# Kernel tuning notes

Hardware: AMD Instinct MI355X
Metric: run time of the kernel (lower is better)

The kernel has to match this reference:

```python
import jax, jax.numpy as jnp
import numpy as np

N = 100000   # nodes
E = 1600000  # edges
D = 256      # emb_dim
H = 512      # 2*emb_dim hidden in GIN MLP
L = 5        # num_layer
NUM_NODE_TYPES = 300
EDGE_FEAT = 7


def setup_inputs() -> dict:
    key = jax.random.key(0)
    ks = jax.random.split(key, 16)
    s = 0.05
    return {
        "x": jax.random.randint(ks[0], (N, 1), 0, NUM_NODE_TYPES, dtype=jnp.int32),
        "edge_index": jax.random.randint(ks[1], (2, E), 0, N, dtype=jnp.int32),
        "edge_attr": jax.random.normal(ks[2], (E, EDGE_FEAT), dtype=jnp.float32),
        "batch": jnp.zeros((N,), dtype=jnp.int32),
        "node_emb": jax.random.normal(ks[3], (NUM_NODE_TYPES, D), dtype=jnp.float32) * s,
        "We": jax.random.normal(ks[4], (L, EDGE_FEAT, D), dtype=jnp.float32) * s,
        "be": jnp.zeros((L, D), dtype=jnp.float32),
        "W1": jax.random.normal(ks[5], (L, D, H), dtype=jnp.float32) * s,
        "b1": jnp.zeros((L, H), dtype=jnp.float32),
        "g1": jnp.ones((L, H), dtype=jnp.float32),
        "bt1": jnp.zeros((L, H), dtype=jnp.float32),
        "W2": jax.random.normal(ks[6], (L, H, D), dtype=jnp.float32) * s,
        "b2": jnp.zeros((L, D), dtype=jnp.float32),
        "eps": jnp.zeros((L,), dtype=jnp.float32),
        "g_bn": jnp.ones((L, D), dtype=jnp.float32),
        "b_bn": jnp.zeros((L, D), dtype=jnp.float32),
    }


def _batchnorm(z, g, b):
    # training-mode BN over the node dim, biased variance, eps=1e-5 (torch default)
    mu = jnp.mean(z, axis=0)
    var = jnp.mean((z - mu) ** 2, axis=0)
    return (z - mu) * jax.lax.rsqrt(var + 1e-5) * g + b


def reference(x, edge_index, edge_attr, batch, node_emb, We, be, W1, b1, g1, bt1,
              W2, b2, eps, g_bn, b_bn):
    src, dst = edge_index[0], edge_index[1]
    h = node_emb[x[:, 0]]                      # [N, D]
    n = h.shape[0]
    for l in range(L):
        edge_emb = edge_attr @ We[l] + be[l]   # [E, D]
        msg = jax.nn.relu(h[src] + edge_emb)   # gather + elementwise message
        agg = jax.ops.segment_sum(msg, dst, num_segments=n)  # scatter-add
        z = (1.0 + eps[l]) * h + agg
        z = jax.nn.relu(_batchnorm(z @ W1[l] + b1[l], g1[l], bt1[l])) @ W2[l] + b2[l]
        z = _batchnorm(z, g_bn[l], b_bn[l])
        h = jax.nn.relu(z) if l != L - 1 else z  # relu on all but last; dropout p=0
    return h  # JK='last'
```

## Files before the change

### kernel.cpp

```cpp
#include <hip/hip_runtime.h>
#include <hip/hip_bf16.h>

#define N_NODES 100000
#define N_EDGES 1600000
#define DIM 256
#define HID 512
#define NLAYERS 5
#define MTILES 782

typedef unsigned short u16;
typedef unsigned int u32;
typedef short s16x8 __attribute__((ext_vector_type(8)));
typedef float f32x4 __attribute__((ext_vector_type(4)));

__device__ __forceinline__ float b2f_(u16 u) {
  union { unsigned i; float f; } v;
  v.i = ((unsigned)u) << 16;
  return v.f;
}
__device__ __forceinline__ u16 f2b_(float f) {
  __hip_bfloat16 h = __float2bfloat16(f);
  return *reinterpret_cast<u16*>(&h);
}
__device__ __forceinline__ int pk2_(u16 lo, u16 hi) {
  return (int)(((u32)hi << 16) | (u32)lo);
}
__device__ __forceinline__ int4 bn_pack_(int4 raw, const float* __restrict__ scl,
                                         const float* __restrict__ sft) {
  const u16* rp = (const u16*)&raw;
  u16 o[8];
#pragma unroll
  for (int q = 0; q < 8; ++q) {
    float v = fmaf(b2f_(rp[q]), scl[q], sft[q]);
    o[q] = f2b_(fmaxf(v, 0.f));
  }
  return make_int4(pk2_(o[0], o[1]), pk2_(o[2], o[3]), pk2_(o[4], o[5]), pk2_(o[6], o[7]));
}

__device__ __forceinline__ void gl16_(const u16* g, u16* l) {
  __builtin_amdgcn_global_load_lds(
      (const __attribute__((address_space(1))) void*)g,
      (__attribute__((address_space(3))) void*)l, 16, 0, 0);
}

__device__ __forceinline__ int lds_off(int row, int g) {
  return row * 32 + (((g ^ (row >> 1)) & 3) << 3);
}

__global__ void k_fill(float* out, int n, float val) {
  int i = blockIdx.x * 256 + threadIdx.x;
  if (i < n) out[i] = val;
}

__global__ void k_zero(float* p, int n) {
  int i = blockIdx.x * 256 + threadIdx.x;
  if (i < n) p[i] = 0.f;
}

__global__ void k_zeroi(int* p, int n) {
  int i = blockIdx.x * 256 + threadIdx.x;
  if (i < n) p[i] = 0;
}

__global__ void k_gather(const int* x0, const int* x3, const float* emb, float* h) {
  int idx = blockIdx.x * 256 + threadIdx.x;
  int n = idx >> 8, d = idx & 255;
  int t = x0[n] + x3[n];
  h[idx] = emb[(size_t)t * DIM + d];
}

__global__ void k_hist(const int* __restrict__ dst, int* __restrict__ deg) {
  int e = blockIdx.x * 256 + threadIdx.x;
  if (e < N_EDGES) atomicAdd(&deg[dst[e]], 1);
}

__global__ void k_scan1(const int* __restrict__ deg, int* __restrict__ offs,
                        int* __restrict__ bsum) {
  __shared__ int sm[256];
  int tid = threadIdx.x;
  int i = blockIdx.x * 256 + tid;
  int v = (i < N_NODES) ? deg[i] : 0;
  sm[tid] = v;
  __syncthreads();
  for (int d = 1; d < 256; d <<= 1) {
    int t = (tid >= d) ? sm[tid - d] : 0;
    __syncthreads();
    sm[tid] += t;
    __syncthreads();
  }
  if (i < N_NODES) offs[i] = sm[tid] - v;
  if (tid == 0) bsum[blockIdx.x] = sm[255];
}

__global__ void k_scan2(int* __restrict__ bsum, int nb) {
  __shared__ int sm[512];
  int tid = threadIdx.x;
  int v = (tid < nb) ? bsum[tid] : 0;
  sm[tid] = v;
  __syncthreads();
  for (int d = 1; d < 512; d <<= 1) {
    int t = (tid >= d) ? sm[tid - d] : 0;
    __syncthreads();
    sm[tid] += t;
    __syncthreads();
  }
  if (tid < nb) bsum[tid] = sm[tid] - v;
}

__global__ void k_scan3(int* __restrict__ offs, const int* __restrict__ bsum,
                        int* __restrict__ cur) {
  int i = blockIdx.x * 256 + threadIdx.x;
  if (i < N_NODES) {
    offs[i] += bsum[blockIdx.x];
    cur[i] = 0;
  }
  if (i == 0) offs[N_NODES] = N_EDGES;
}

__global__ void k_fillcsr(const int* __restrict__ dst, const int* __restrict__ srcarr,
                          const float* __restrict__ ea, const int* __restrict__ offs,
                          int* __restrict__ cur, int* __restrict__ elist,
                          float* __restrict__ eaperm) {
  int e = blockIdx.x * 256 + threadIdx.x;
  if (e < N_EDGES) {
    int d = dst[e];
    int p = offs[d] + atomicAdd(&cur[d], 1);
    elist[p] = srcarr[e];
    const float* s = ea + (size_t)e * 7;
    float* o = eaperm + (size_t)p * 7;
#pragma unroll
    for (int k = 0; k < 7; ++k) o[k] = s[k];
  }
}

template <int BNIN>
__global__ __launch_bounds__(256) void k_agg(
    const float* __restrict__ hin, const float* __restrict__ eap,
    const int* __restrict__ csr, const int* __restrict__ offs,
    const float* __restrict__ We, const float* __restrict__ be,
    const float* __restrict__ eps_l, const float* __restrict__ scl2,
    const float* __restrict__ sft2, u16* __restrict__ zh, u16* __restrict__ zl) {
  const int lane = threadIdx.x & 63;
  const int n = blockIdx.x * 4 + (threadIdx.x >> 6);
  const int c0 = lane * 4;
  float w[7][4];
#pragma unroll
  for (int k = 0; k < 7; ++k) {
    f32x4 t = *(const f32x4*)&We[k * DIM + c0];
    w[k][0] = t[0]; w[k][1] = t[1]; w[k][2] = t[2]; w[k][3] = t[3];
  }
  const f32x4 bev = *(const f32x4*)&be[c0];
  f32x4 sv, fv;
  if (BNIN) { sv = *(const f32x4*)&scl2[c0]; fv = *(const f32x4*)&sft2[c0]; }
  const f32x4 hn = *(const f32x4*)&hin[(size_t)n * DIM + c0];
  const float e1p = 1.0f + eps_l[0];
  float acc[4];
#pragma unroll
  for (int q = 0; q < 4; ++q) {
    float hv = hn[q];
    if (BNIN) hv = fmaxf(fmaf(hv, sv[q], fv[q]), 0.f);
    acc[q] = e1p * hv;
  }

  auto msg = [&](const f32x4& hs, const float* a) {
#pragma unroll
    for (int q = 0; q < 4; ++q) {
      float hv = hs[q];
      if (BNIN) hv = fmaxf(fmaf(hv, sv[q], fv[q]), 0.f);
      float t = bev[q];
#pragma unroll
      for (int k = 0; k < 7; ++k) t = fmaf(a[k], w[k][q], t);
      acc[q] += fmaxf(hv + t, 0.f);
    }
  };

  const int eb = offs[n], ee = offs[n + 1];
  for (int base = eb; base < ee; base += 64) {
    const int m = min(64, ee - base);
    const int cs = csr[base + min(lane, m - 1)];
    int e = 0;
    for (; e + 4 <= m; e += 4) {
      const int s0 = __shfl(cs, e);
      const int s1 = __shfl(cs, e + 1);
      const int s2 = __shfl(cs, e + 2);
      const int s3 = __shfl(cs, e + 3);
      const f32x4 h0 = *(const f32x4*)&hin[(size_t)s0 * DIM + c0];
      const f32x4 h1 = *(const f32x4*)&hin[(size_t)s1 * DIM + c0];
      const f32x4 h2 = *(const f32x4*)&hin[(size_t)s2 * DIM + c0];
      const f32x4 h3 = *(const f32x4*)&hin[(size_t)s3 * DIM + c0];
      const float* p0 = eap + (size_t)(base + e) * 7;
      float a0[7], a1[7], a2[7], a3[7];
#pragma unroll
      for (int k = 0; k < 7; ++k) {
        a0[k] = p0[k]; a1[k] = p0[7 + k]; a2[k] = p0[14 + k]; a3[k] = p0[21 + k];
      }
      msg(h0, a0);
      msg(h1, a1);
      msg(h2, a2);
      msg(h3, a3);
    }
    for (; e < m; ++e) {
      const int s0 = __shfl(cs, e);
      const f32x4 h0 = *(const f32x4*)&hin[(size_t)s0 * DIM + c0];
      const float* p0 = eap + (size_t)(base + e) * 7;
      float a0[7];
#pragma unroll
      for (int k = 0; k < 7; ++k) a0[k] = p0[k];
      msg(h0, a0);
    }
  }
  ushort4 zh4, zl4;
#pragma unroll
  for (int q = 0; q < 4; ++q) {
    u16 hh = f2b_(acc[q]);
    float lo = acc[q] - b2f_(hh);
    ((u16*)&zh4)[q] = hh;
    ((u16*)&zl4)[q] = f2b_(lo);
  }
  *(ushort4*)&zh[(size_t)n * DIM + c0] = zh4;
  *(ushort4*)&zl[(size_t)n * DIM + c0] = zl4;
}

template <int K, int NC>
__global__ void k_wconv(const float* __restrict__ W, u16* __restrict__ Wth,
                        u16* __restrict__ Wtl) {
  int idx = blockIdx.x * 256 + threadIdx.x;
  int n = idx / K, k = idx - n * K;
  float w = W[(size_t)k * NC + n];
  u16 hh = f2b_(w);
  Wth[idx] = hh;
  Wtl[idx] = f2b_(w - b2f_(hh));
}

__global__ void k_bnprep(const float* __restrict__ sum, const float* __restrict__ sq,
                         const float* __restrict__ g, const float* __restrict__ bt,
                         float* __restrict__ scl, float* __restrict__ sft, int n) {
  int j = blockIdx.x * 256 + threadIdx.x;
  if (j < n) {
    const float invN = 1.0f / 100000.0f;
    float mu = sum[j] * invN;
    float var = fmaf(-mu, mu, sq[j] * invN);
    float s = g[j] * rsqrtf(var + 1e-5f);
    scl[j] = s;
    sft[j] = fmaf(-mu, s, bt[j]);
  }
}

template <int K, int NC, int NA, int OBF, int BN1A>
__global__ __launch_bounds__(256) void k_mgemm(
    const u16* __restrict__ Ah, const u16* __restrict__ Al,
    const u16* __restrict__ Bth, const u16* __restrict__ Btl,
    const float* __restrict__ bias, void* __restrict__ Ov,
    float* __restrict__ colsum, float* __restrict__ colsq,
    const float* __restrict__ ascl, const float* __restrict__ asft) {
  __shared__ u16 As[NA * 128 * 32];
  __shared__ u16 Bs[2 * 128 * 32];
  constexpr int NT = NC / 128;
  const int nwg = MTILES * NT;
  const int bid = blockIdx.x;
  const int q = nwg >> 3, r = nwg & 7;
  const int xcd = bid & 7, pos = bid >> 3;
  const int lidx = (xcd < r) ? (xcd * (q + 1) + pos)
                             : (r * (q + 1) + (xcd - r) * q + pos);
  const int mt = lidx / NT;
  const int m0 = mt * 128;
  const int n0 = (lidx - mt * NT) * 128;

  const int tid = threadIdx.x;
  const int lane = tid & 63;
  const int wv = tid >> 6;
  const int wr = (wv >> 1) * 64;
  const int wc = (wv & 1) * 64;
  const int lr = lane & 15;
  const int g = lane >> 4;
  const int sr = tid >> 1;
  const int sc = (tid & 1) * 16;
  const int ga = min(m0 + sr, N_NODES - 1);
  const int grow16 = lane >> 2;
  const int glc = (lane & 3) ^ ((lane >> 3) & 3);

  const f32x4 z4 = {0.f, 0.f, 0.f, 0.f};
  f32x4 acc[4][4];
#pragma unroll
  for (int i = 0; i < 4; ++i)
#pragma unroll
    for (int j = 0; j < 4; ++j) acc[i][j] = z4;

  for (int k0 = 0; k0 < K; k0 += 32) {
    int4 a0, a1;
    if (NA == 1) {
      const u16* srcp = Ah + (size_t)ga * K + k0 + sc;
      a0 = *(const int4*)(srcp);
      a1 = *(const int4*)(srcp + 8);
      if (BN1A) {
        a0 = bn_pack_(a0, ascl + k0 + sc, asft + k0 + sc);
        a1 = bn_pack_(a1, ascl + k0 + sc + 8, asft + k0 + sc + 8);
      }
    }
    __syncthreads();
    if (NA == 2) {
      const u16* gbase;
      u16* lbase;
      int rbase, rclamp;
      if (wv == 0)      { gbase = Ah;  lbase = As;        rbase = m0; rclamp = N_NODES - 1; }
      else if (wv == 1) { gbase = Al;  lbase = As + 4096; rbase = m0; rclamp = N_NODES - 1; }
      else if (wv == 2) { gbase = Bth; lbase = Bs;        rbase = n0; rclamp = 0x7fffffff; }
      else              { gbase = Btl; lbase = Bs + 4096; rbase = n0; rclamp = 0x7fffffff; }
#pragma unroll
      for (int c = 0; c < 8; ++c) {
        int gr = min(rbase + c * 16 + grow16, rclamp);
        gl16_(gbase + (size_t)gr * K + k0 + glc * 8, lbase + c * 512);
      }
    } else {
      const int x = (sr >> 1) & 3;
      const int lc0 = (tid & 1) * 2;
      *(int4*)&As[sr * 32 + ((lc0 ^ x) << 3)] = a0;
      *(int4*)&As[sr * 32 + (((lc0 + 1) ^ x) << 3)] = a1;
      const u16* gbase = (wv >> 1) ? Btl : Bth;
      u16* lbase = (wv >> 1) ? Bs + 4096 : Bs;
#pragma unroll
      for (int cc = 0; cc < 4; ++cc) {
        int c = (wv & 1) * 4 + cc;
        int gr = n0 + c * 16 + grow16;
        gl16_(gbase + (size_t)gr * K + k0 + glc * 8, lbase + c * 512);
      }
    }
    __syncthreads();

    s16x8 aF[NA][4], bF[2][4];
#pragma unroll
    for (int i = 0; i < 4; ++i) {
      aF[0][i] = *reinterpret_cast<const s16x8*>(&As[lds_off(wr + i * 16 + lr, g)]);
      if (NA == 2)
        aF[1][i] = *reinterpret_cast<const s16x8*>(&As[4096 + lds_off(wr + i * 16 + lr, g)]);
      bF[0][i] = *reinterpret_cast<const s16x8*>(&Bs[lds_off(wc + i * 16 + lr, g)]);
      bF[1][i] = *reinterpret_cast<const s16x8*>(&Bs[4096 + lds_off(wc + i * 16 + lr, g)]);
    }
#pragma unroll
    for (int i = 0; i < 4; ++i)
#pragma unroll
      for (int j = 0; j < 4; ++j) {
        acc[i][j] =
            __builtin_amdgcn_mfma_f32_16x16x32_bf16(aF[0][i], bF[0][j], acc[i][j], 0, 0, 0);
        acc[i][j] =
            __builtin_amdgcn_mfma_f32_16x16x32_bf16(aF[0][i], bF[1][j], acc[i][j], 0, 0, 0);
        if (NA == 2)
          acc[i][j] =
              __builtin_amdgcn_mfma_f32_16x16x32_bf16(aF[1][i], bF[0][j], acc[i][j], 0, 0, 0);
      }
  }

  float bj[4];
#pragma unroll
  for (int j = 0; j < 4; ++j) bj[j] = bias[n0 + wc + j * 16 + lr];
  float ls[4] = {0.f, 0.f, 0.f, 0.f}, lq[4] = {0.f, 0.f, 0.f, 0.f};
#pragma unroll
  for (int i = 0; i < 4; ++i) {
    const int row0 = m0 + wr + i * 16 + (lane >> 4) * 4;
#pragma unroll
    for (int r2 = 0; r2 < 4; ++r2) {
      const int grow = row0 + r2;
      if (grow < N_NODES) {
        const size_t o = (size_t)grow * NC + n0 + wc + lr;
#pragma unroll
        for (int j = 0; j < 4; ++j) {
          float v = acc[i][j][r2] + bj[j];
          ls[j] += v;
          lq[j] = fmaf(v, v, lq[j]);
          if (OBF) ((u16*)Ov)[o + j * 16] = f2b_(v);
          else ((float*)Ov)[o + j * 16] = v;
        }
      }
    }
  }
#pragma unroll
  for (int j = 0; j < 4; ++j) {
    float s = ls[j], q2 = lq[j];
    s += __shfl_xor(s, 16); q2 += __shfl_xor(q2, 16);
    s += __shfl_xor(s, 32); q2 += __shfl_xor(q2, 32);
    if ((lane >> 4) == 0) {
      unsafeAtomicAdd(&colsum[n0 + wc + j * 16 + lr], s);
      unsafeAtomicAdd(&colsq[n0 + wc + j * 16 + lr], q2);
    }
  }
}

__global__ void k_bn(const void* Y, int y_bf, const float* sum, const float* sq,
                     const float* g, const float* b, int NC_mask,
                     void* O, int o_bf, int do_relu) {
  int idx = blockIdx.x * 256 + threadIdx.x;
  int j = idx & NC_mask;
  const float invN = 1.0f / 100000.0f;
  float mu = sum[j] * invN;
  float var = fmaf(-mu, mu, sq[j] * invN);
  float v = y_bf ? b2f_(((const u16*)Y)[idx]) : ((const float*)Y)[idx];
  v = fmaf((v - mu) * rsqrtf(var + 1e-5f), g[j], b[j]);
  if (do_relu) v = fmaxf(v, 0.f);
  if (o_bf) ((u16*)O)[idx] = f2b_(v);
  else ((float*)O)[idx] = v;
}

extern "C" void kernel_launch(void* const* d_in, const int* in_sizes, int n_in,
                              void* d_out, int out_size, void* d_ws, size_t ws_size,
                              hipStream_t stream) {
  float* out = (float*)d_out;

  const int expected[16] = {100000, 3200000, 11200000, 100000, 76800, 8960, 1280,
                            655360, 2560, 2560, 2560, 655360, 1280, 5, 1280, 1280};
  float sentinel = 0.f;
  if (n_in != 16) sentinel = 60.f;
  else
    for (int i = 0; i < 16; ++i)
      if (in_sizes[i] != expected[i]) { sentinel = 100.f + (float)i; break; }
  if (sentinel == 0.f && out_size != N_NODES * DIM) sentinel = 90.f;

  const size_t ND = (size_t)N_NODES * DIM;
  const size_t NH = (size_t)N_NODES * HID;
  const size_t base = 4096 * sizeof(float);
  const size_t need_base = base + 2 * ND * sizeof(float) + NH * sizeof(u16);
  if (sentinel == 0.f && ws_size < need_base) sentinel = 77.f;
  if (sentinel != 0.f) {
    k_fill<<<(out_size + 255) / 256, 256, 0, stream>>>(out, out_size, sentinel);
    return;
  }

  float* stats = (float*)d_ws;
  float* sum1 = stats;
  float* sq1 = sum1 + HID;
  float* sum2 = sq1 + HID;
  float* sq2 = sum2 + DIM;
  float* scl1 = stats + 1536;
  float* sft1 = scl1 + HID;
  float* scl2 = sft1 + HID;
  float* sft2 = scl2 + DIM;
  float* bufA = stats + 4096;
  float* bufB = bufA + ND;
  u16* Y1 = (u16*)(bufB + ND);

  const size_t csr_ints =
      (size_t)N_NODES + (size_t)(N_NODES + 1) + 512 + 1 + (size_t)N_EDGES;
  const size_t csr_bytes = csr_ints * sizeof(int) + (size_t)N_EDGES * 7 * sizeof(float);
  const int csr_tail = ws_size >= need_base + csr_bytes;
  int* degc = csr_tail ? (int*)((char*)d_ws + need_base) : (int*)Y1;
  int* offs = degc + N_NODES;
  int* bsum = offs + N_NODES + 1;
  int* elist = bsum + 512 + 1;
  float* eaperm = (float*)(elist + N_EDGES);
  const int NB_N = (N_NODES + 255) / 256;
  const int NB_E = N_EDGES / 256;

  const int* x0 = (const int*)d_in[0];
  const int* ei = (const int*)d_in[1];
  const float* ea = (const float*)d_in[2];
  const int* x3 = (const int*)d_in[3];
  const float* emb = (const float*)d_in[4];
  const float* We = (const float*)d_in[5];
  const float* be = (const float*)d_in[6];
  const float* W1 = (const float*)d_in[7];
  const float* b1 = (const float*)d_in[8];
  const float* g1 = (const float*)d_in[9];
  const float* bt1 = (const float*)d_in[10];
  const float* W2 = (const float*)d_in[11];
  const float* b2 = (const float*)d_in[12];
  const float* eps = (const float*)d_in[13];
  const float* g_bn = (const float*)d_in[14];
  const float* b_bn = (const float*)d_in[15];

  const int* srcs = ei;
  const int* dsts = ei + N_EDGES;

  const int gridND = (int)(ND / 256);

  auto build_csr = [&]() {
    k_zeroi<<<NB_N, 256, 0, stream>>>(degc, N_NODES);
    k_hist<<<NB_E, 256, 0, stream>>>(dsts, degc);
    k_scan1<<<NB_N, 256, 0, stream>>>(degc, offs, bsum);
    k_scan2<<<1, 512, 0, stream>>>(bsum, NB_N);
    k_scan3<<<NB_N, 256, 0, stream>>>(offs, bsum, degc);
    k_fillcsr<<<NB_E, 256, 0, stream>>>(dsts, srcs, ea, offs, degc, elist, eaperm);
  };

  k_gather<<<gridND, 256, 0, stream>>>(x0, x3, emb, bufA);
  if (csr_tail) build_csr();

  float* bufs[2] = {bufA, bufB};
  int p = 0;
  for (int l = 0; l < NLAYERS; ++l) {
    float* IN = bufs[p];
    float* ZB = bufs[1 - p];
    u16* zh = (u16*)ZB;
    u16* zl = zh + ND;
    u16* Wth = (u16*)IN;
    u16* Wtl = Wth + (size_t)DIM * HID;

    if (!csr_tail) build_csr();
    k_zero<<<6, 256, 0, stream>>>(stats, 1536);

    if (l == 0)
      k_agg<0><<<N_NODES / 4, 256, 0, stream>>>(IN, eaperm, elist, offs,
                                                We + (size_t)l * 7 * DIM,
                                                be + (size_t)l * DIM, eps + l,
                                                nullptr, nullptr, zh, zl);
    else
      k_agg<1><<<N_NODES / 4, 256, 0, stream>>>(IN, eaperm, elist, offs,
                                                We + (size_t)l * 7 * DIM,
                                                be + (size_t)l * DIM, eps + l,
                                                scl2, sft2, zh, zl);

    k_wconv<DIM, HID><<<(DIM * HID) / 256, 256, 0, stream>>>(
        W1 + (size_t)l * DIM * HID, Wth, Wtl);
    k_mgemm<DIM, HID, 2, 1, 0><<<MTILES * (HID / 128), 256, 0, stream>>>(
        zh, zl, Wth, Wtl, b1 + (size_t)l * HID, Y1, sum1, sq1, nullptr, nullptr);
    k_bnprep<<<2, 256, 0, stream>>>(sum1, sq1, g1 + (size_t)l * HID,
                                    bt1 + (size_t)l * HID, scl1, sft1, HID);

    k_wconv<HID, DIM><<<(DIM * HID) / 256, 256, 0, stream>>>(
        W2 + (size_t)l * HID * DIM, Wth, Wtl);
    k_mgemm<HID, DIM, 1, 0, 1><<<MTILES * (DIM / 128), 256, 0, stream>>>(
        Y1, nullptr, Wth, Wtl, b2 + (size_t)l * DIM, ZB, sum2, sq2, scl1, sft1);

    if (l != NLAYERS - 1)
      k_bnprep<<<1, 256, 0, stream>>>(sum2, sq2, g_bn + (size_t)l * DIM,
                                      b_bn + (size_t)l * DIM, scl2, sft2, DIM);
    else
      k_bn<<<gridND, 256, 0, stream>>>(ZB, 0, sum2, sq2, g_bn + (size_t)l * DIM,
                                       b_bn + (size_t)l * DIM, DIM - 1, out, 0, 0);
    p ^= 1;
  }
}
```

Baseline: 2.878 ms.

## Double-buffer LDS tiles in split-bf16 MFMA GEMM to overlap loads with compute

Restructures the GEMM k-loop to use two LDS buffers for A and B tiles. The next tile's global-to-LDS DMA and register loads are issued before the current tile's MFMAs, so memory latency can hide behind compute. This also drops one barrier per iteration. In exchange the kernel uses twice the shared memory, which can lower occupancy, and holds more live registers across the MFMA block.

```diff
diff --git a/kernel.cpp b/kernel.cpp
--- a/kernel.cpp
+++ b/kernel.cpp
@@ -253,18 +253,20 @@
     const float* __restrict__ bias, void* __restrict__ Ov,
     float* __restrict__ colsum, float* __restrict__ colsq,
     const float* __restrict__ ascl, const float* __restrict__ asft) {
-  __shared__ u16 As[NA * 128 * 32];
-  __shared__ u16 Bs[2 * 128 * 32];
-  constexpr int NT = NC / 128;
-  const int nwg = MTILES * NT;
+  constexpr int PL = 128 * 32;
+  constexpr int NT = K / 32;
+  __shared__ u16 As[2 * NA * PL];
+  __shared__ u16 Bs[2 * 2 * PL];
+  constexpr int NTL = NC / 128;
+  const int nwg = MTILES * NTL;
   const int bid = blockIdx.x;
   const int q = nwg >> 3, r = nwg & 7;
   const int xcd = bid & 7, pos = bid >> 3;
   const int lidx = (xcd < r) ? (xcd * (q + 1) + pos)
                              : (r * (q + 1) + (xcd - r) * q + pos);
-  const int mt = lidx / NT;
+  const int mt = lidx / NTL;
   const int m0 = mt * 128;
-  const int n0 = (lidx - mt * NT) * 128;
+  const int n0 = (lidx - mt * NTL) * 128;
 
   const int tid = threadIdx.x;
   const int lane = tid & 63;
@@ -279,45 +281,24 @@
   const int grow16 = lane >> 2;
   const int glc = (lane & 3) ^ ((lane >> 3) & 3);
 
-  const f32x4 z4 = {0.f, 0.f, 0.f, 0.f};
-  f32x4 acc[4][4];
-#pragma unroll
-  for (int i = 0; i < 4; ++i)
-#pragma unroll
-    for (int j = 0; j < 4; ++j) acc[i][j] = z4;
-
-  for (int k0 = 0; k0 < K; k0 += 32) {
-    int4 a0, a1;
-    if (NA == 1) {
-      const u16* srcp = Ah + (size_t)ga * K + k0 + sc;
-      a0 = *(const int4*)(srcp);
-      a1 = *(const int4*)(srcp + 8);
-      if (BN1A) {
-        a0 = bn_pack_(a0, ascl + k0 + sc, asft + k0 + sc);
-        a1 = bn_pack_(a1, ascl + k0 + sc + 8, asft + k0 + sc + 8);
-      }
-    }
-    __syncthreads();
+  auto stage_dma = [&](int kt, int buf) {
+    const int k0 = kt * 32;
     if (NA == 2) {
       const u16* gbase;
       u16* lbase;
       int rbase, rclamp;
-      if (wv == 0)      { gbase = Ah;  lbase = As;        rbase = m0; rclamp = N_NODES - 1; }
-      else if (wv == 1) { gbase = Al;  lbase = As + 4096; rbase = m0; rclamp = N_NODES - 1; }
-      else if (wv == 2) { gbase = Bth; lbase = Bs;        rbase = n0; rclamp = 0x7fffffff; }
-      else              { gbase = Btl; lbase = Bs + 4096; rbase = n0; rclamp = 0x7fffffff; }
+      if (wv == 0)      { gbase = Ah;  lbase = As + buf * (NA * PL);      rbase = m0; rclamp = N_NODES - 1; }
+      else if (wv == 1) { gbase = Al;  lbase = As + buf * (NA * PL) + PL; rbase = m0; rclamp = N_NODES - 1; }
+      else if (wv == 2) { gbase = Bth; lbase = Bs + buf * (2 * PL);       rbase = n0; rclamp = 0x7fffffff; }
+      else              { gbase = Btl; lbase = Bs + buf * (2 * PL) + PL;  rbase = n0; rclamp = 0x7fffffff; }
 #pragma unroll
       for (int c = 0; c < 8; ++c) {
         int gr = min(rbase + c * 16 + grow16, rclamp);
         gl16_(gbase + (size_t)gr * K + k0 + glc * 8, lbase + c * 512);
       }
     } else {
-      const int x = (sr >> 1) & 3;
-      const int lc0 = (tid & 1) * 2;
-      *(int4*)&As[sr * 32 + ((lc0 ^ x) << 3)] = a0;
-      *(int4*)&As[sr * 32 + (((lc0 + 1) ^ x) << 3)] = a1;
       const u16* gbase = (wv >> 1) ? Btl : Bth;
-      u16* lbase = (wv >> 1) ? Bs + 4096 : Bs;
+      u16* lbase = Bs + buf * (2 * PL) + ((wv >> 1) ? PL : 0);
 #pragma unroll
       for (int cc = 0; cc < 4; ++cc) {
         int c = (wv & 1) * 4 + cc;
@@ -325,16 +306,60 @@
         gl16_(gbase + (size_t)gr * K + k0 + glc * 8, lbase + c * 512);
       }
     }
-    __syncthreads();
-
+  };
+  auto a_write = [&](int4 a0, int4 a1, int buf) {
+    const int x = (sr >> 1) & 3;
+    const int lc0 = (tid & 1) * 2;
+    u16* ab = As + buf * PL;
+    *(int4*)&ab[sr * 32 + ((lc0 ^ x) << 3)] = a0;
+    *(int4*)&ab[sr * 32 + (((lc0 + 1) ^ x) << 3)] = a1;
+  };
+  auto a_load = [&](int kt, int4& a0, int4& a1) {
+    const u16* srcp = Ah + (size_t)ga * K + kt * 32 + sc;
+    a0 = *(const int4*)(srcp);
+    a1 = *(const int4*)(srcp + 8);
+  };
+  auto a_bn = [&](int4& a0, int4& a1, int kt) {
+    if (BN1A) {
+      const int k0 = kt * 32;
+      a0 = bn_pack_(a0, ascl + k0 + sc, asft + k0 + sc);
+      a1 = bn_pack_(a1, ascl + k0 + sc + 8, asft + k0 + sc + 8);
+    }
+  };
+
+  const f32x4 z4 = {0.f, 0.f, 0.f, 0.f};
+  f32x4 acc[4][4];
+#pragma unroll
+  for (int i = 0; i < 4; ++i)
+#pragma unroll
+    for (int j = 0; j < 4; ++j) acc[i][j] = z4;
+
+  if (NA == 1) {
+    int4 p0, p1;
+    a_load(0, p0, p1);
+    a_bn(p0, p1, 0);
+    a_write(p0, p1, 0);
+  }
+  stage_dma(0, 0);
+  __syncthreads();
+
+  int cur = 0;
+  for (int t = 0; t < NT; ++t) {
+    const u16* ap = As + cur * (NA * PL);
+    const u16* bp = Bs + cur * (2 * PL);
     s16x8 aF[NA][4], bF[2][4];
 #pragma unroll
     for (int i = 0; i < 4; ++i) {
-      aF[0][i] = *reinterpret_cast<const s16x8*>(&As[lds_off(wr + i * 16 + lr, g)]);
+      aF[0][i] = *reinterpret_cast<const s16x8*>(&ap[lds_off(wr + i * 16 + lr, g)]);
       if (NA == 2)
-        aF[1][i] = *reinterpret_cast<const s16x8*>(&As[4096 + lds_off(wr + i * 16 + lr, g)]);
-      bF[0][i] = *reinterpret_cast<const s16x8*>(&Bs[lds_off(wc + i * 16 + lr, g)]);
-      bF[1][i] = *reinterpret_cast<const s16x8*>(&Bs[4096 + lds_off(wc + i * 16 + lr, g)]);
+        aF[1][i] = *reinterpret_cast<const s16x8*>(&ap[PL + lds_off(wr + i * 16 + lr, g)]);
+      bF[0][i] = *reinterpret_cast<const s16x8*>(&bp[lds_off(wc + i * 16 + lr, g)]);
+      bF[1][i] = *reinterpret_cast<const s16x8*>(&bp[PL + lds_off(wc + i * 16 + lr, g)]);
+    }
+    int4 n0r, n1r;
+    if (t + 1 < NT) {
+      if (NA == 1) a_load(t + 1, n0r, n1r);
+      stage_dma(t + 1, cur ^ 1);
     }
 #pragma unroll
     for (int i = 0; i < 4; ++i)
@@ -348,6 +373,12 @@
           acc[i][j] =
               __builtin_amdgcn_mfma_f32_16x16x32_bf16(aF[1][i], bF[0][j], acc[i][j], 0, 0, 0);
       }
+    if (NA == 1 && t + 1 < NT) {
+      a_bn(n0r, n1r, t + 1);
+      a_write(n0r, n1r, cur ^ 1);
+    }
+    __syncthreads();
+    cur ^= 1;
   }
 
   float bj[4];
```

Measured after the change: 3.005 ms. 1.04x slower.
